# Kernel optimization log

Measured on AMD Instinct MI355X. Metric: run time of the kernel, lower is better.

## Reference

```python
import jax, jax.numpy as jnp
import numpy as np

B, T, C = 2, 2048, 1024
NH, HD = 16, 64  # n_head, head_dim (qk == vo)


def setup_inputs() -> dict:
    key = jax.random.key(0)
    ks = jax.random.split(key, 5)
    scale = 1.0 / np.sqrt(C)
    return {
        "x": jax.random.normal(ks[0], (B, T, C), dtype=jnp.float32),
        "Wq": jax.random.normal(ks[1], (C, C), dtype=jnp.float32) * scale,
        "Wk": jax.random.normal(ks[2], (C, C), dtype=jnp.float32) * scale,
        "Wv": jax.random.normal(ks[3], (C, C), dtype=jnp.float32) * scale,
        "Wo": jax.random.normal(ks[4], (C, C), dtype=jnp.float32) * scale,
    }


def reference(x, Wq, Wk, Wv, Wo):
    # torch Linear: y = x @ W.T (weights stored [out, in])
    q = (x @ Wq.T).reshape(B, T, NH, HD).transpose(0, 2, 1, 3)  # [B,H,T,D]
    k = (x @ Wk.T).reshape(B, T, NH, HD).transpose(0, 2, 1, 3)
    v = (x @ Wv.T).reshape(B, T, NH, HD).transpose(0, 2, 1, 3)
    att = jnp.einsum("bhqd,bhkd->bhqk", q, k) * (1.0 / np.sqrt(HD))
    causal = jnp.tril(jnp.ones((T, T), dtype=bool))
    att = jnp.where(causal[None, None], att, -jnp.inf)
    att = jax.nn.softmax(att, axis=-1)
    y = jnp.einsum("bhqk,bhkd->bhqd", att, v)  # [B,H,T,D]
    y = y.transpose(0, 2, 1, 3).reshape(B, T, NH * HD)
    return y @ Wo.T  # dropout p=0 -> identity
```

## Files before the change

kernel.cpp:

```cpp
#include <hip/hip_runtime.h>
#include <hip/hip_bf16.h>
#include <cstdint>
#include <cstddef>
#include <cmath>

#define B_  2
#define T_  2048
#define C_  1024
#define NH_ 16
#define HD_ 64

typedef __bf16 bf16;
typedef bf16  bf16x8 __attribute__((ext_vector_type(8)));
typedef bf16  bf16x4 __attribute__((ext_vector_type(4)));
typedef float f32x4  __attribute__((ext_vector_type(4)));

#define MFMA16(a, b, c) __builtin_amdgcn_mfma_f32_16x16x32_bf16((a), (b), (c), 0, 0, 0)

__device__ __forceinline__ void gld_lds16(const bf16* g, bf16* lds_base_uniform) {
    __builtin_amdgcn_global_load_lds(
        (const __attribute__((address_space(1))) uint32_t*)g,
        (__attribute__((address_space(3))) uint32_t*)lds_base_uniform,
        16, 0, 0);
}

__global__ __launch_bounds__(256) void cast_f32_bf16(const float* __restrict__ in,
                                                     bf16* __restrict__ out, int n4) {
    int i = blockIdx.x * 256 + threadIdx.x;
    if (i < n4) {
        float4 v = ((const float4*)in)[i];
        bf16x4 o = { (bf16)v.x, (bf16)v.y, (bf16)v.z, (bf16)v.w };
        ((bf16x4*)out)[i] = o;
    }
}

__global__ __launch_bounds__(256) void cast_weights(const float* __restrict__ Wq,
                                                    const float* __restrict__ Wk,
                                                    const float* __restrict__ Wv,
                                                    const float* __restrict__ Wo,
                                                    bf16* __restrict__ Wqk,
                                                    bf16* __restrict__ Wvb,
                                                    bf16* __restrict__ Wob) {
    const int i = blockIdx.x * 256 + threadIdx.x;
    const int nw4 = C_ * C_ / 4;
    float4 q = ((const float4*)Wq)[i];
    float4 k = ((const float4*)Wk)[i];
    float4 v = ((const float4*)Wv)[i];
    float4 o = ((const float4*)Wo)[i];
    ((bf16x4*)Wqk)[i]       = bf16x4{ (bf16)q.x, (bf16)q.y, (bf16)q.z, (bf16)q.w };
    ((bf16x4*)Wqk)[nw4 + i] = bf16x4{ (bf16)k.x, (bf16)k.y, (bf16)k.z, (bf16)k.w };
    ((bf16x4*)Wvb)[i]       = bf16x4{ (bf16)v.x, (bf16)v.y, (bf16)v.z, (bf16)v.w };
    ((bf16x4*)Wob)[i]       = bf16x4{ (bf16)o.x, (bf16)o.y, (bf16)o.z, (bf16)o.w };
}

__device__ __forceinline__ void gemm_tile(bf16* As, bf16* Bs,
                                          const bf16* __restrict__ A,
                                          const bf16* __restrict__ W,
                                          bf16* __restrict__ Y,
                                          int N, int K, int m0, int n0) {
    const int tid  = threadIdx.x;
    const int lane = tid & 63;
    const int w    = tid >> 6;
    const int ml   = lane & 15;
    const int quad = lane >> 4;
    const int wm   = (w >> 1) * 64;
    const int wn   = (w & 1) * 64;
    const int sr   = lane >> 2;
    const int sc   = lane & 3;

    f32x4 acc[4][4] = {};

    for (int k0 = 0; k0 < K; k0 += 32) {
        __syncthreads();
#pragma unroll
        for (int ei = 0; ei < 2; ++ei) {
            const int e = w * 2 + ei;
            gld_lds16(A + (size_t)(m0 + e * 16 + sr) * K + k0 + sc * 8, &As[e * 512]);
            gld_lds16(W + (size_t)(n0 + e * 16 + sr) * K + k0 + sc * 8, &Bs[e * 512]);
        }
        __builtin_amdgcn_s_waitcnt(0);
        __syncthreads();

        bf16x8 af[4], bfr[4];
#pragma unroll
        for (int t = 0; t < 4; ++t) {
            af[t]  = *(const bf16x8*)&As[(wm + t * 16 + ml) * 32 + quad * 8];
            bfr[t] = *(const bf16x8*)&Bs[(wn + t * 16 + ml) * 32 + quad * 8];
        }
#pragma unroll
        for (int mt = 0; mt < 4; ++mt)
#pragma unroll
            for (int nt = 0; nt < 4; ++nt)
                acc[mt][nt] = MFMA16(af[mt], bfr[nt], acc[mt][nt]);
    }

#pragma unroll
    for (int mt = 0; mt < 4; ++mt)
#pragma unroll
        for (int nt = 0; nt < 4; ++nt)
#pragma unroll
            for (int r = 0; r < 4; ++r) {
                const int row = m0 + wm + mt * 16 + quad * 4 + r;
                const int col = n0 + wn + nt * 16 + ml;
                Y[(size_t)row * N + col] = (bf16)acc[mt][nt][r];
            }
}

__global__ __launch_bounds__(256) void proj_fused(const bf16* __restrict__ xb,
                                                  const bf16* __restrict__ Wqk,
                                                  const bf16* __restrict__ Wvb,
                                                  bf16* __restrict__ QKb,
                                                  bf16* __restrict__ VtT) {
    __shared__ __align__(16) bf16 As[128 * 32];
    __shared__ __align__(16) bf16 Bs[128 * 32];
    const int bid = blockIdx.x;
    if (bid < 512) {
        gemm_tile(As, Bs, xb, Wqk, QKb, 2048, 1024, (bid >> 4) * 128, (bid & 15) * 128);
    } else {
        const int b2 = bid - 512;
        gemm_tile(As, Bs, Wvb, xb, VtT, 4096, 1024, (b2 >> 5) * 128, (b2 & 31) * 128);
    }
}

__global__ __launch_bounds__(256) void gemm_wo(const bf16* __restrict__ A,
                                               const bf16* __restrict__ W,
                                               float* __restrict__ Y) {
    __shared__ __align__(16) bf16 As[64 * 32];
    __shared__ __align__(16) bf16 Bs[128 * 32];
    const int tid  = threadIdx.x;
    const int lane = tid & 63;
    const int w    = tid >> 6;
    const int ml   = lane & 15;
    const int quad = lane >> 4;
    const int wm   = (w >> 1) * 32;
    const int wn   = (w & 1) * 64;
    const int m0   = blockIdx.y * 64;
    const int n0   = blockIdx.x * 128;
    const int sr   = lane >> 2;
    const int sc   = lane & 3;

    f32x4 acc[2][4] = {};

    for (int k0 = 0; k0 < 1024; k0 += 32) {
        __syncthreads();
        gld_lds16(A + (size_t)(m0 + w * 16 + sr) * 1024 + k0 + sc * 8, &As[w * 512]);
#pragma unroll
        for (int ei = 0; ei < 2; ++ei) {
            const int e = w * 2 + ei;
            gld_lds16(W + (size_t)(n0 + e * 16 + sr) * 1024 + k0 + sc * 8, &Bs[e * 512]);
        }
        __builtin_amdgcn_s_waitcnt(0);
        __syncthreads();

        bf16x8 af[2], bfr[4];
#pragma unroll
        for (int t = 0; t < 2; ++t)
            af[t] = *(const bf16x8*)&As[(wm + t * 16 + ml) * 32 + quad * 8];
#pragma unroll
        for (int t = 0; t < 4; ++t)
            bfr[t] = *(const bf16x8*)&Bs[(wn + t * 16 + ml) * 32 + quad * 8];
#pragma unroll
        for (int mt = 0; mt < 2; ++mt)
#pragma unroll
            for (int nt = 0; nt < 4; ++nt)
                acc[mt][nt] = MFMA16(af[mt], bfr[nt], acc[mt][nt]);
    }

#pragma unroll
    for (int mt = 0; mt < 2; ++mt)
#pragma unroll
        for (int nt = 0; nt < 4; ++nt)
#pragma unroll
            for (int r = 0; r < 4; ++r) {
                const int row = m0 + wm + mt * 16 + quad * 4 + r;
                const int col = n0 + wn + nt * 16 + ml;
                Y[(size_t)row * 1024 + col] = acc[mt][nt][r];
            }
}

__global__ __launch_bounds__(256, 3) void attn_mfma(const bf16* __restrict__ QKb,
                                                    const bf16* __restrict__ VtT,
                                                    bf16* __restrict__ Pbuf,
                                                    float* __restrict__ Lbuf) {
    const int bid  = blockIdx.x;
    const int hb   = bid & 31;
    const int s    = 79 - (bid >> 5);
    int qt, chunk;
    if (s < 8)       { qt = s;                   chunk = 0; }
    else if (s < 24) { qt = 8  + ((s - 8) >> 1); chunk = (s - 8) & 1; }
    else if (s < 48) { qt = 16 + (s - 24) / 3;   chunk = (s - 24) % 3; }
    else             { qt = 24 + ((s - 48) >> 2); chunk = (s - 48) & 3; }
    const int h = hb >> 1, b = hb & 1;

    const int tid  = threadIdx.x;
    const int lane = tid & 63;
    const int w    = tid >> 6;
    const int ml   = lane & 15;
    const int quad = lane >> 4;

    __shared__ __align__(16) bf16 Ks[2][4096];
    __shared__ __align__(16) bf16 Vs[2][4096];
    __shared__ __align__(16) bf16 Ps[4][16 * 72];

    const bf16* Qbase = QKb + (size_t)b * T_ * 2048 + (size_t)h * HD_;
    const bf16* Kbase = Qbase + 1024;
    const bf16* Vbase = VtT + (size_t)h * HD_ * 4096 + (size_t)b * T_;

    const float C1  = 0.1803368801111f;
    const float C2M = 28.8539008178f;

    const int qrow = qt * 64 + w * 16 + ml;
    bf16x8 qf[2];
#pragma unroll
    for (int ks = 0; ks < 2; ++ks)
        qf[ks] = *(const bf16x8*)(Qbase + (size_t)qrow * 2048 + ks * 32 + quad * 8);

    f32x4 o_acc[4] = {};
    f32x4 l_acc = {};
    bf16x8 onesf;
#pragma unroll
    for (int j = 0; j < 8; ++j) onesf[j] = (bf16)1.0f;

    const int sr = lane >> 2, sc = lane & 3;
    bf16* ps = &Ps[w][0];

    const int ktbase  = chunk * 8;
    const int nrounds = min(8, qt + 1 - ktbase);

    auto stage = [&](int ktg, int buf) {
        const int k0 = ktg * 64;
#pragma unroll
        for (int ei = 0; ei < 2; ++ei) {
            const int e = w * 2 + ei;
            const int r = (e & 3) * 16 + sr;
            const int ch = (e >> 2) * 32 + sc * 8;
            gld_lds16(Kbase + (size_t)(k0 + r) * 2048 + ch, &Ks[buf][e * 512]);
            gld_lds16(Vbase + (size_t)r * 4096 + k0 + ch, &Vs[buf][e * 512]);
        }
    };

    stage(ktbase, 0);

    for (int j = 0; j < nrounds; ++j) {
        const int cur = j & 1;
        const int ktg = ktbase + j;
        const int k0  = ktg * 64;

        asm volatile("s_barrier" ::: "memory");
        if (j + 1 < nrounds) {
            stage(ktg + 1, cur ^ 1);
            asm volatile("s_waitcnt vmcnt(4)" ::: "memory");
        } else {
            asm volatile("s_waitcnt vmcnt(0)" ::: "memory");
        }
        asm volatile("s_barrier" ::: "memory");

#pragma unroll
        for (int nt = 0; nt < 4; ++nt) {
            f32x4 sacc = {};
#pragma unroll
            for (int ks = 0; ks < 2; ++ks) {
                bf16x8 kf = *(const bf16x8*)&Ks[cur][ks * 2048 + (nt * 16 + ml) * 32 + quad * 8];
                sacc = MFMA16(qf[ks], kf, sacc);
            }
            const int kg = k0 + nt * 16 + ml;
#pragma unroll
            for (int r = 0; r < 4; ++r) {
                float arg = fmaf(sacc[r], C1, -C2M);
                if (ktg == qt) {
                    const int qg = qt * 64 + w * 16 + quad * 4 + r;
                    if (kg > qg) arg = -1e30f;
                }
                ps[(quad * 4 + r) * 72 + nt * 16 + ml] = (bf16)exp2f(arg);
            }
        }

#pragma unroll
        for (int ks = 0; ks < 2; ++ks) {
            bf16x8 pf = *(const bf16x8*)&ps[ml * 72 + ks * 32 + quad * 8];
            l_acc = MFMA16(pf, onesf, l_acc);
#pragma unroll
            for (int nt = 0; nt < 4; ++nt) {
                bf16x8 vf = *(const bf16x8*)&Vs[cur][ks * 2048 + (nt * 16 + ml) * 32 + quad * 8];
                o_acc[nt] = MFMA16(pf, vf, o_acc[nt]);
            }
        }
    }

    const int slotIdx = hb * 80 + s;
    bf16* pb = Pbuf + (size_t)slotIdx * 4096;
#pragma unroll
    for (int r = 0; r < 4; ++r) {
        const int prow = w * 16 + quad * 4 + r;
#pragma unroll
        for (int nt = 0; nt < 4; ++nt)
            pb[prow * 64 + nt * 16 + ml] = (bf16)o_acc[nt][r];
        if (ml == 0)
            Lbuf[slotIdx * 64 + prow] = l_acc[r];
    }
}

__global__ __launch_bounds__(256) void attn_merge(const bf16* __restrict__ Pbuf,
                                                  const float* __restrict__ Lbuf,
                                                  bf16* __restrict__ Ab) {
    const int gid = blockIdx.x;
    const int qt  = gid >> 5;
    const int hb  = gid & 31;
    const int h = hb >> 1, b = hb & 1;
    int s0;
    if (qt < 8)       s0 = qt;
    else if (qt < 16) s0 = 8 + (qt - 8) * 2;
    else if (qt < 24) s0 = 24 + (qt - 16) * 3;
    else              s0 = 48 + (qt - 24) * 4;
    const int nch = (qt + 8) >> 3;

    const int tid = threadIdx.x;
    const int row = tid >> 2;
    const int cg  = (tid & 3) * 16;

    float acc[16] = {};
    float lsum = 0.f;
    for (int c = 0; c < nch; ++c) {
        const int slotIdx = hb * 80 + s0 + c;
        lsum += Lbuf[slotIdx * 64 + row];
        const bf16* pb = Pbuf + (size_t)slotIdx * 4096 + row * 64 + cg;
        bf16x8 v0 = *(const bf16x8*)pb;
        bf16x8 v1 = *(const bf16x8*)(pb + 8);
#pragma unroll
        for (int j = 0; j < 8; ++j) { acc[j] += (float)v0[j]; acc[8 + j] += (float)v1[j]; }
    }
    const float rcl = 1.0f / lsum;
    bf16x8 o0, o1;
#pragma unroll
    for (int j = 0; j < 8; ++j) { o0[j] = (bf16)(acc[j] * rcl); o1[j] = (bf16)(acc[8 + j] * rcl); }
    bf16* dst = Ab + (size_t)(b * T_ + qt * 64 + row) * 1024 + h * 64 + cg;
    *(bf16x8*)dst = o0;
    *(bf16x8*)(dst + 8) = o1;
}

extern "C" void kernel_launch(void* const* d_in, const int* in_sizes, int n_in,
                              void* d_out, int out_size, void* d_ws, size_t ws_size,
                              hipStream_t stream) {
    const float* x  = (const float*)d_in[0];
    const float* Wq = (const float*)d_in[1];
    const float* Wk = (const float*)d_in[2];
    const float* Wv = (const float*)d_in[3];
    const float* Wo = (const float*)d_in[4];
    float* out = (float*)d_out;

    const size_t n_x = (size_t)B_ * T_ * C_;
    const size_t n_w = (size_t)C_ * C_;

    bf16* xb   = (bf16*)d_ws;
    bf16* Wqk  = xb + n_x;
    bf16* Wvb  = Wqk + 2 * n_w;
    bf16* Wob  = Wvb + n_w;
    bf16* QKb  = Wob + n_w;
    bf16* VtT  = QKb + 2 * n_x;
    bf16* Ab   = VtT + n_x;
    bf16* Pbuf = Ab + n_x;
    float* Lbuf = (float*)(Pbuf + (size_t)2560 * 4096);

    cast_f32_bf16<<<(int)(n_x / 4 / 256), 256, 0, stream>>>(x, xb, (int)(n_x / 4));
    cast_weights<<<(int)(n_w / 4 / 256), 256, 0, stream>>>(Wq, Wk, Wv, Wo, Wqk, Wvb, Wob);

    proj_fused<<<768, 256, 0, stream>>>(xb, Wqk, Wvb, QKb, VtT);

    attn_mfma<<<2560, 256, 0, stream>>>(QKb, VtT, Pbuf, Lbuf);
    attn_merge<<<1024, 256, 0, stream>>>(Pbuf, Lbuf, Ab);

    gemm_wo<<<dim3(1024 / 128, 4096 / 64), 256, 0, stream>>>(Ab, Wob, out);
}
```

Baseline: 189.7 us.

## Single-buffer V in attention, raise occupancy, fold softmax scale into Wq

V tiles now use a single LDS buffer that is loaded at the start of each round. K stays double-buffered, and split waitcnt/barrier points let the QK^T/exp phase overlap the V load. This shrinks LDS per block so launch bounds can go from 3 to 4 blocks per CU. The softmax scale is folded into the Wq bf16 cast and the constant exponent offset is dropped, removing an FMA per score. The risks are less prefetch depth for V, and larger unnormalised exp values that depend on the merge step to normalise them.

New measurement: 186.4 us. Within noise of the previous version (-1.7%).

```diff
diff --git a/kernel.cpp b/kernel.cpp
--- a/kernel.cpp
+++ b/kernel.cpp
@@ -41,13 +41,15 @@
                                                     bf16* __restrict__ Wqk,
                                                     bf16* __restrict__ Wvb,
                                                     bf16* __restrict__ Wob) {
+    const float C1 = 0.1803368801111f;
     const int i = blockIdx.x * 256 + threadIdx.x;
     const int nw4 = C_ * C_ / 4;
     float4 q = ((const float4*)Wq)[i];
     float4 k = ((const float4*)Wk)[i];
     float4 v = ((const float4*)Wv)[i];
     float4 o = ((const float4*)Wo)[i];
-    ((bf16x4*)Wqk)[i]       = bf16x4{ (bf16)q.x, (bf16)q.y, (bf16)q.z, (bf16)q.w };
+    ((bf16x4*)Wqk)[i]       = bf16x4{ (bf16)(q.x * C1), (bf16)(q.y * C1),
+                                      (bf16)(q.z * C1), (bf16)(q.w * C1) };
     ((bf16x4*)Wqk)[nw4 + i] = bf16x4{ (bf16)k.x, (bf16)k.y, (bf16)k.z, (bf16)k.w };
     ((bf16x4*)Wvb)[i]       = bf16x4{ (bf16)v.x, (bf16)v.y, (bf16)v.z, (bf16)v.w };
     ((bf16x4*)Wob)[i]       = bf16x4{ (bf16)o.x, (bf16)o.y, (bf16)o.z, (bf16)o.w };
@@ -178,7 +180,7 @@
             }
 }
 
-__global__ __launch_bounds__(256, 3) void attn_mfma(const bf16* __restrict__ QKb,
+__global__ __launch_bounds__(256, 4) void attn_mfma(const bf16* __restrict__ QKb,
                                                     const bf16* __restrict__ VtT,
                                                     bf16* __restrict__ Pbuf,
                                                     float* __restrict__ Lbuf) {
@@ -199,16 +201,13 @@
     const int quad = lane >> 4;
 
     __shared__ __align__(16) bf16 Ks[2][4096];
-    __shared__ __align__(16) bf16 Vs[2][4096];
+    __shared__ __align__(16) bf16 Vs[4096];
     __shared__ __align__(16) bf16 Ps[4][16 * 72];
 
     const bf16* Qbase = QKb + (size_t)b * T_ * 2048 + (size_t)h * HD_;
     const bf16* Kbase = Qbase + 1024;
     const bf16* Vbase = VtT + (size_t)h * HD_ * 4096 + (size_t)b * T_;
 
-    const float C1  = 0.1803368801111f;
-    const float C2M = 28.8539008178f;
-
     const int qrow = qt * 64 + w * 16 + ml;
     bf16x8 qf[2];
 #pragma unroll
@@ -227,7 +226,7 @@
     const int ktbase  = chunk * 8;
     const int nrounds = min(8, qt + 1 - ktbase);
 
-    auto stage = [&](int ktg, int buf) {
+    auto stageK = [&](int ktg, int buf) {
         const int k0 = ktg * 64;
 #pragma unroll
         for (int ei = 0; ei < 2; ++ei) {
@@ -235,26 +234,21 @@
             const int r = (e & 3) * 16 + sr;
             const int ch = (e >> 2) * 32 + sc * 8;
             gld_lds16(Kbase + (size_t)(k0 + r) * 2048 + ch, &Ks[buf][e * 512]);
-            gld_lds16(Vbase + (size_t)r * 4096 + k0 + ch, &Vs[buf][e * 512]);
         }
     };
-
-    stage(ktbase, 0);
-
-    for (int j = 0; j < nrounds; ++j) {
-        const int cur = j & 1;
-        const int ktg = ktbase + j;
-        const int k0  = ktg * 64;
-
-        asm volatile("s_barrier" ::: "memory");
-        if (j + 1 < nrounds) {
-            stage(ktg + 1, cur ^ 1);
-            asm volatile("s_waitcnt vmcnt(4)" ::: "memory");
-        } else {
-            asm volatile("s_waitcnt vmcnt(0)" ::: "memory");
-        }
-        asm volatile("s_barrier" ::: "memory");
-
+    auto stageV = [&](int ktg) {
+        const int k0 = ktg * 64;
+#pragma unroll
+        for (int ei = 0; ei < 2; ++ei) {
+            const int e = w * 2 + ei;
+            const int r = (e & 3) * 16 + sr;
+            const int ch = (e >> 2) * 32 + sc * 8;
+            gld_lds16(Vbase + (size_t)r * 4096 + k0 + ch, &Vs[e * 512]);
+        }
+    };
+
+    auto phase1 = [&](int cur, int ktg) {
+        const int k0 = ktg * 64;
 #pragma unroll
         for (int nt = 0; nt < 4; ++nt) {
             f32x4 sacc = {};
@@ -266,7 +260,7 @@
             const int kg = k0 + nt * 16 + ml;
 #pragma unroll
             for (int r = 0; r < 4; ++r) {
-                float arg = fmaf(sacc[r], C1, -C2M);
+                float arg = sacc[r];
                 if (ktg == qt) {
                     const int qg = qt * 64 + w * 16 + quad * 4 + r;
                     if (kg > qg) arg = -1e30f;
@@ -274,16 +268,44 @@
                 ps[(quad * 4 + r) * 72 + nt * 16 + ml] = (bf16)exp2f(arg);
             }
         }
-
+    };
+
+    auto phase2 = [&]() {
 #pragma unroll
         for (int ks = 0; ks < 2; ++ks) {
             bf16x8 pf = *(const bf16x8*)&ps[ml * 72 + ks * 32 + quad * 8];
             l_acc = MFMA16(pf, onesf, l_acc);
 #pragma unroll
             for (int nt = 0; nt < 4; ++nt) {
-                bf16x8 vf = *(const bf16x8*)&Vs[cur][ks * 2048 + (nt * 16 + ml) * 32 + quad * 8];
+                bf16x8 vf = *(const bf16x8*)&Vs[ks * 2048 + (nt * 16 + ml) * 32 + quad * 8];
                 o_acc[nt] = MFMA16(pf, vf, o_acc[nt]);
             }
+        }
+    };
+
+    stageK(ktbase, 0);
+
+    for (int j = 0; j < nrounds; ++j) {
+        const int cur = j & 1;
+        const int ktg = ktbase + j;
+
+        asm volatile("s_barrier" ::: "memory");
+        stageV(ktg);
+        if (j + 1 < nrounds) {
+            stageK(ktg + 1, cur ^ 1);
+            asm volatile("s_waitcnt vmcnt(4)" ::: "memory");
+            asm volatile("s_barrier" ::: "memory");
+            phase1(cur, ktg);
+            asm volatile("s_waitcnt vmcnt(2)" ::: "memory");
+            asm volatile("s_barrier" ::: "memory");
+            phase2();
+        } else {
+            asm volatile("s_waitcnt vmcnt(2)" ::: "memory");
+            asm volatile("s_barrier" ::: "memory");
+            phase1(cur, ktg);
+            asm volatile("s_waitcnt vmcnt(0)" ::: "memory");
+            asm volatile("s_barrier" ::: "memory");
+            phase2();
         }
     }
 
```
